# Kernel tuning notes

Measured on AMD Instinct MI355X. Metric: run time of the kernel, lower is better.

## Reference

```python
import jax, jax.numpy as jnp
import numpy as np

B, C, L, H, W = 2, 64, 8, 32, 32

def setup_inputs() -> dict:
    key = jax.random.key(0)
    ks = jax.random.split(key, 10)
    return {
        "q": jax.random.normal(ks[0], (B, C, L, H, W), dtype=jnp.float32),
        "k": jax.random.normal(ks[1], (B, C, L, H, W), dtype=jnp.float32),
        "v": jax.random.normal(ks[2], (B, C, L, H, W), dtype=jnp.float32),
        "wq": jax.random.normal(ks[3], (C,), dtype=jnp.float32) * 0.1,
        "bq": jax.random.normal(ks[4], (1,), dtype=jnp.float32) * 0.1,
        "wk": jax.random.normal(ks[5], (C,), dtype=jnp.float32) * 0.1,
        "bk": jax.random.normal(ks[6], (1,), dtype=jnp.float32) * 0.1,
        "wv": jax.random.normal(ks[7], (C, 3 * C), dtype=jnp.float32) * 0.1,
        "bv": jax.random.normal(ks[8], (C,), dtype=jnp.float32) * 0.1,
        "gamma_x": jax.random.normal(ks[9], (1,), dtype=jnp.float32) * 0.1,
    }


def reference(q, k, v, wq, bq, wk, bk, wv, bv, gamma_x):
    # q,k,v: [B,C,L,H,W]; 1x1x1 conv3d == channel contraction
    Bq, Cq, Lq, Hq, Wq = q.shape
    N = Lq * Hq * Wq
    qf = q.reshape(Bq, Cq, N)
    kf = k.reshape(Bq, Cq, N)
    vf = v.reshape(Bq, Cq, N)
    # query/key conv: C -> 1 channel => [B, N]
    pq = jnp.einsum('bcn,c->bn', qf, wq) + bq  # [B,N]
    pk = jnp.einsum('bcn,c->bn', kf, wk) + bk  # [B,N]
    # energy = bmm([B,N,1],[B,1,N]) = outer product -> [B,N,N]
    energy = pq[:, :, None] * pk[:, None, :]
    attn = jax.nn.softmax(energy, axis=-1)  # softmax over key index n
    # value path: cat(v, q, k) along channels -> [B,3C,N], then 3C -> C conv
    val = jnp.concatenate([vf, qf, kf], axis=1)
    pv = jnp.einsum('bdn,cd->bcn', val, wv) + bv[None, :, None]  # [B,C,N]
    # out[b,c,m] = sum_n pv[b,c,n] * attn[b,m,n]  (bmm with attn^T)
    out = jnp.einsum('bcn,bmn->bcm', pv, attn).reshape(Bq, Cq, Lq, Hq, Wq)
    return gamma_x * out + v
```

## Files before the change

### kernel.cpp

```cpp
#include <hip/hip_runtime.h>


typedef __attribute__((ext_vector_type(8))) __bf16 bf16x8;
typedef __attribute__((ext_vector_type(4))) float  f32x4;

#define NN 8192
#define CC 64
#define NJ 48

__global__ __launch_bounds__(256) void pqpk_kernel(
    const float* __restrict__ q, const float* __restrict__ k,
    const float* __restrict__ wq, const float* __restrict__ bq,
    const float* __restrict__ wk, const float* __restrict__ bk,
    float* __restrict__ pq, float* __restrict__ pk)
{
    int t = threadIdx.x, lane = t & 63, wid = t >> 6;
    int b  = blockIdx.x >> 6;
    int n  = ((blockIdx.x & 63) << 7) + ((wid & 1) << 6) + lane;

    const float* src = (wid < 2) ? q : k;
    const float* wgt = (wid < 2) ? wq : wk;
    float bias       = (wid < 2) ? bq[0] : bk[0];
    float* dst       = (wid < 2) ? pq : pk;

    const float* sp = src + (size_t)b * CC * NN + n;
    float a = 0.f;
    #pragma unroll 8
    for (int d = 0; d < 64; d++) a = fmaf(sp[(size_t)d * NN], wgt[d], a);
    dst[b * NN + n] = a + bias;
}

__global__ __launch_bounds__(256) void fused_kernel(
    const float* __restrict__ q, const float* __restrict__ k,
    const float* __restrict__ v, const float* __restrict__ wv,
    const float* __restrict__ bv, const float* __restrict__ pk,
    float* __restrict__ G, float* __restrict__ T)
{
    __shared__ __align__(16) __bf16 val_sT[64][200];
    __shared__ __align__(16) __bf16 pv_s[64][72];
    __shared__ __align__(16) __bf16 V_s[NJ][72];

    int t = threadIdx.x, lane = t & 63, wid = t >> 6;
    int quad = lane >> 4, cl = lane & 15;
    int b   = blockIdx.x >> 6;
    int nb0 = (blockIdx.x & 63) << 7;
    size_t bo = (size_t)b * CC * NN;

    bf16x8 wvA[6];
    const float* wr = wv + (size_t)(wid * 16 + cl) * 192;
    #pragma unroll
    for (int ks = 0; ks < 6; ks++) {
        f32x4 a0 = *(const f32x4*)(wr + ks * 32 + quad * 8);
        f32x4 a1 = *(const f32x4*)(wr + ks * 32 + quad * 8 + 4);
        #pragma unroll
        for (int e = 0; e < 4; e++) {
            wvA[ks][e]     = (__bf16)a0[e];
            wvA[ks][4 + e] = (__bf16)a1[e];
        }
    }
    float bvr[4];
    #pragma unroll
    for (int r = 0; r < 4; r++) bvr[r] = bv[wid * 16 + quad * 4 + r];

    f32x4 accG[3];
    #pragma unroll
    for (int jt = 0; jt < 3; jt++) accG[jt] = (f32x4){0.f, 0.f, 0.f, 0.f};
    float tsum = 0.f;

    for (int s = 0; s < 2; s++) {
        int n0 = nb0 + s * 64;
        if (wid < 3) {
            int dt = t >> 3, no = t & 7;
            int dbase = dt * 8;
            const float* src = (dbase < 64)  ? (v + bo + (size_t)dbase * NN)
                             : (dbase < 128) ? (q + bo + (size_t)(dbase - 64) * NN)
                                             : (k + bo + (size_t)(dbase - 128) * NN);
            float tile[8][8];
            #pragma unroll
            for (int dd = 0; dd < 8; dd++) {
                f32x4 x0 = *(const f32x4*)(src + (size_t)dd * NN + n0 + no * 8);
                f32x4 x1 = *(const f32x4*)(src + (size_t)dd * NN + n0 + no * 8 + 4);
                #pragma unroll
                for (int e = 0; e < 4; e++) { tile[dd][e] = x0[e]; tile[dd][4 + e] = x1[e]; }
            }
            #pragma unroll
            for (int nn = 0; nn < 8; nn++) {
                bf16x8 wb;
                #pragma unroll
                for (int dd = 0; dd < 8; dd++) wb[dd] = (__bf16)tile[dd][nn];
                *(bf16x8*)&val_sT[no * 8 + nn][dbase] = wb;
            }
        } else {
            float tv = pk[b * NN + n0 + lane];
            float tp = 1.f;
            #pragma unroll
            for (int j = 0; j < NJ; j++) {
                V_s[j][lane] = (__bf16)tp;
                tp *= tv;
            }
        }
        __syncthreads();

        f32x4 accP[4];
        #pragma unroll
        for (int nt = 0; nt < 4; nt++) accP[nt] = (f32x4){0.f, 0.f, 0.f, 0.f};
        #pragma unroll
        for (int ks = 0; ks < 6; ks++)
            #pragma unroll
            for (int nt = 0; nt < 4; nt++) {
                bf16x8 bfr = *(const bf16x8*)&val_sT[nt * 16 + cl][ks * 32 + quad * 8];
                accP[nt] = __builtin_amdgcn_mfma_f32_16x16x32_bf16(wvA[ks], bfr, accP[nt], 0, 0, 0);
            }

        #pragma unroll
        for (int nt = 0; nt < 4; nt++)
            #pragma unroll
            for (int r = 0; r < 4; r++)
                pv_s[wid * 16 + quad * 4 + r][nt * 16 + cl] = (__bf16)(accP[nt][r] + bvr[r]);

        #pragma unroll
        for (int k0 = 0; k0 < 64; k0 += 32) {
            bf16x8 a = *(const bf16x8*)&pv_s[wid * 16 + cl][k0 + quad * 8];
            #pragma unroll
            for (int jt = 0; jt < 3; jt++) {
                bf16x8 bfr = *(const bf16x8*)&V_s[jt * 16 + cl][k0 + quad * 8];
                accG[jt] = __builtin_amdgcn_mfma_f32_16x16x32_bf16(a, bfr, accG[jt], 0, 0, 0);
            }
        }
        if (t < NJ) {
            #pragma unroll
            for (int h = 0; h < 8; h++) {
                bf16x8 vv = *(const bf16x8*)&V_s[t][h * 8];
                #pragma unroll
                for (int e = 0; e < 8; e++) tsum += (float)vv[e];
            }
        }
        __syncthreads();
    }

    #pragma unroll
    for (int jt = 0; jt < 3; jt++)
        #pragma unroll
        for (int r = 0; r < 4; r++)
            atomicAdd(&G[((size_t)b * CC + wid * 16 + quad * 4 + r) * NJ + jt * 16 + cl],
                      accG[jt][r]);
    if (t < NJ) atomicAdd(&T[b * NJ + t], tsum);
}

__global__ __launch_bounds__(256) void eval_kernel(
    const float* __restrict__ pq, const float* __restrict__ G,
    const float* __restrict__ T, const float* __restrict__ v,
    const float* __restrict__ gamma, float* __restrict__ out)
{
    int t = threadIdx.x;
    int b   = blockIdx.x >> 8;
    int mch = (blockIdx.x >> 3) & 31;
    int cg  = blockIdx.x & 7;

    int m = mch * 256 + t;
    float s = pq[b * NN + m];
    const float* Gr = G + ((size_t)b * CC + cg * 8) * NJ;
    const float* Tr = T + b * NJ;

    float acc[8];
    #pragma unroll
    for (int c = 0; c < 8; c++) acc[c] = 0.f;
    float z = 0.f, cj = 1.f;
    #pragma unroll
    for (int j = 0; j < NJ; j++) {
        if (j > 0) cj *= s * (1.0f / (float)j);
        z = fmaf(cj, Tr[j], z);
        #pragma unroll
        for (int c = 0; c < 8; c++) acc[c] = fmaf(cj, Gr[c * NJ + j], acc[c]);
    }
    float gz = gamma[0] / z;

    #pragma unroll
    for (int c = 0; c < 8; c++) {
        size_t idx = ((size_t)b * CC + cg * 8 + c) * NN + m;
        out[idx] = fmaf(gz, acc[c], v[idx]);
    }
}

extern "C" void kernel_launch(void* const* d_in, const int* in_sizes, int n_in,
                              void* d_out, int out_size, void* d_ws, size_t ws_size,
                              hipStream_t stream)
{
    const float* q     = (const float*)d_in[0];
    const float* k     = (const float*)d_in[1];
    const float* v     = (const float*)d_in[2];
    const float* wq    = (const float*)d_in[3];
    const float* bq    = (const float*)d_in[4];
    const float* wk    = (const float*)d_in[5];
    const float* bk    = (const float*)d_in[6];
    const float* wv    = (const float*)d_in[7];
    const float* bv    = (const float*)d_in[8];
    const float* gamma = (const float*)d_in[9];

    float* pqw = (float*)d_ws;
    float* pkw = pqw + 2 * NN;
    float* Gw  = pkw + 2 * NN;
    float* Tw  = Gw + 2 * CC * NJ;

    hipMemsetAsync(Gw, 0, (2 * CC * NJ + 2 * NJ) * sizeof(float), stream);
    pqpk_kernel<<<128, 256, 0, stream>>>(q, k, wq, bq, wk, bk, pqw, pkw);
    fused_kernel<<<128, 256, 0, stream>>>(q, k, v, wv, bv, pkw, Gw, Tw);
    eval_kernel<<<512, 256, 0, stream>>>(pqw, Gw, Tw, v, gamma, (float*)d_out);
}
```

Before: 98.50 us.

## Fold workspace zeroing into pqpk kernel and double grid sizes for parallelism

Removes the separate memset launch by having the projection kernel zero the G/T accumulators. The projection kernel now splits the channel reduction across four waves and combines partial sums in shared memory. The fused kernel processes one 64-column tile per block over 256 blocks instead of looping over two tiles in 128 blocks. The aim is to fill more CUs on the chip and cut launch overhead, at the cost of twice as many atomic adds into G and T.

```diff
diff --git a/kernel.cpp b/kernel.cpp
--- a/kernel.cpp
+++ b/kernel.cpp
@@ -12,22 +12,37 @@
     const float* __restrict__ q, const float* __restrict__ k,
     const float* __restrict__ wq, const float* __restrict__ bq,
     const float* __restrict__ wk, const float* __restrict__ bk,
-    float* __restrict__ pq, float* __restrict__ pk)
-{
+    float* __restrict__ pq, float* __restrict__ pk, float* __restrict__ GT)
+{
+    __shared__ float pqp[4][64], pkp[4][64];
+
     int t = threadIdx.x, lane = t & 63, wid = t >> 6;
-    int b  = blockIdx.x >> 6;
-    int n  = ((blockIdx.x & 63) << 7) + ((wid & 1) << 6) + lane;
-
-    const float* src = (wid < 2) ? q : k;
-    const float* wgt = (wid < 2) ? wq : wk;
-    float bias       = (wid < 2) ? bq[0] : bk[0];
-    float* dst       = (wid < 2) ? pq : pk;
-
-    const float* sp = src + (size_t)b * CC * NN + n;
-    float a = 0.f;
-    #pragma unroll 8
-    for (int d = 0; d < 64; d++) a = fmaf(sp[(size_t)d * NN], wgt[d], a);
-    dst[b * NN + n] = a + bias;
+    int b  = blockIdx.x >> 7;
+    int n0 = (blockIdx.x & 127) << 6;
+    int n  = n0 + lane;
+
+    int gid = blockIdx.x * 256 + t;
+    if (gid < 2 * CC * NJ + 2 * NJ) GT[gid] = 0.f;
+
+    size_t bo = (size_t)b * CC * NN + (size_t)(wid * 16) * NN + n;
+    const float* qp = q + bo;
+    const float* kp = k + bo;
+    float aq = 0.f, ak = 0.f;
+    #pragma unroll
+    for (int d = 0; d < 16; d++) {
+        aq = fmaf(qp[(size_t)d * NN], wq[wid * 16 + d], aq);
+        ak = fmaf(kp[(size_t)d * NN], wk[wid * 16 + d], ak);
+    }
+    pqp[wid][lane] = aq;
+    pkp[wid][lane] = ak;
+    __syncthreads();
+
+    if (t < 64)
+        pq[b * NN + n0 + t] = pqp[0][t] + pqp[1][t] + pqp[2][t] + pqp[3][t] + bq[0];
+    else if (t < 128) {
+        int u = t - 64;
+        pk[b * NN + n0 + u] = pkp[0][u] + pkp[1][u] + pkp[2][u] + pkp[3][u] + bk[0];
+    }
 }
 
 __global__ __launch_bounds__(256) void fused_kernel(
@@ -42,8 +57,8 @@
 
     int t = threadIdx.x, lane = t & 63, wid = t >> 6;
     int quad = lane >> 4, cl = lane & 15;
-    int b   = blockIdx.x >> 6;
-    int nb0 = (blockIdx.x & 63) << 7;
+    int b  = blockIdx.x >> 7;
+    int n0 = (blockIdx.x & 127) << 6;
     size_t bo = (size_t)b * CC * NN;
 
     bf16x8 wvA[6];
@@ -62,80 +77,66 @@
     #pragma unroll
     for (int r = 0; r < 4; r++) bvr[r] = bv[wid * 16 + quad * 4 + r];
 
+    if (wid < 3) {
+        int dt = t >> 3, no = t & 7;
+        int dbase = dt * 8;
+        const float* src = (dbase < 64)  ? (v + bo + (size_t)dbase * NN)
+                         : (dbase < 128) ? (q + bo + (size_t)(dbase - 64) * NN)
+                                         : (k + bo + (size_t)(dbase - 128) * NN);
+        float tile[8][8];
+        #pragma unroll
+        for (int dd = 0; dd < 8; dd++) {
+            f32x4 x0 = *(const f32x4*)(src + (size_t)dd * NN + n0 + no * 8);
+            f32x4 x1 = *(const f32x4*)(src + (size_t)dd * NN + n0 + no * 8 + 4);
+            #pragma unroll
+            for (int e = 0; e < 4; e++) { tile[dd][e] = x0[e]; tile[dd][4 + e] = x1[e]; }
+        }
+        #pragma unroll
+        for (int nn = 0; nn < 8; nn++) {
+            bf16x8 wb;
+            #pragma unroll
+            for (int dd = 0; dd < 8; dd++) wb[dd] = (__bf16)tile[dd][nn];
+            *(bf16x8*)&val_sT[no * 8 + nn][dbase] = wb;
+        }
+    } else {
+        float tv = pk[b * NN + n0 + lane];
+        float tp = 1.f;
+        #pragma unroll
+        for (int j = 0; j < NJ; j++) {
+            V_s[j][lane] = (__bf16)tp;
+            tp *= tv;
+        }
+    }
+    __syncthreads();
+
+    f32x4 accP[4];
+    #pragma unroll
+    for (int nt = 0; nt < 4; nt++) accP[nt] = (f32x4){0.f, 0.f, 0.f, 0.f};
+    #pragma unroll
+    for (int ks = 0; ks < 6; ks++)
+        #pragma unroll
+        for (int nt = 0; nt < 4; nt++) {
+            bf16x8 bfr = *(const bf16x8*)&val_sT[nt * 16 + cl][ks * 32 + quad * 8];
+            accP[nt] = __builtin_amdgcn_mfma_f32_16x16x32_bf16(wvA[ks], bfr, accP[nt], 0, 0, 0);
+        }
+
+    #pragma unroll
+    for (int nt = 0; nt < 4; nt++)
+        #pragma unroll
+        for (int r = 0; r < 4; r++)
+            pv_s[wid * 16 + quad * 4 + r][nt * 16 + cl] = (__bf16)(accP[nt][r] + bvr[r]);
+
     f32x4 accG[3];
     #pragma unroll
     for (int jt = 0; jt < 3; jt++) accG[jt] = (f32x4){0.f, 0.f, 0.f, 0.f};
-    float tsum = 0.f;
-
-    for (int s = 0; s < 2; s++) {
-        int n0 = nb0 + s * 64;
-        if (wid < 3) {
-            int dt = t >> 3, no = t & 7;
-            int dbase = dt * 8;
-            const float* src = (dbase < 64)  ? (v + bo + (size_t)dbase * NN)
-                             : (dbase < 128) ? (q + bo + (size_t)(dbase - 64) * NN)
-                                             : (k + bo + (size_t)(dbase - 128) * NN);
-            float tile[8][8];
-            #pragma unroll
-            for (int dd = 0; dd < 8; dd++) {
-                f32x4 x0 = *(const f32x4*)(src + (size_t)dd * NN + n0 + no * 8);
-                f32x4 x1 = *(const f32x4*)(src + (size_t)dd * NN + n0 + no * 8 + 4);
-                #pragma unroll
-                for (int e = 0; e < 4; e++) { tile[dd][e] = x0[e]; tile[dd][4 + e] = x1[e]; }
-            }
-            #pragma unroll
-            for (int nn = 0; nn < 8; nn++) {
-                bf16x8 wb;
-                #pragma unroll
-                for (int dd = 0; dd < 8; dd++) wb[dd] = (__bf16)tile[dd][nn];
-                *(bf16x8*)&val_sT[no * 8 + nn][dbase] = wb;
-            }
-        } else {
-            float tv = pk[b * NN + n0 + lane];
-            float tp = 1.f;
-            #pragma unroll
-            for (int j = 0; j < NJ; j++) {
-                V_s[j][lane] = (__bf16)tp;
-                tp *= tv;
-            }
-        }
-        __syncthreads();
-
-        f32x4 accP[4];
-        #pragma unroll
-        for (int nt = 0; nt < 4; nt++) accP[nt] = (f32x4){0.f, 0.f, 0.f, 0.f};
-        #pragma unroll
-        for (int ks = 0; ks < 6; ks++)
-            #pragma unroll
-            for (int nt = 0; nt < 4; nt++) {
-                bf16x8 bfr = *(const bf16x8*)&val_sT[nt * 16 + cl][ks * 32 + quad * 8];
-                accP[nt] = __builtin_amdgcn_mfma_f32_16x16x32_bf16(wvA[ks], bfr, accP[nt], 0, 0, 0);
-            }
-
-        #pragma unroll
-        for (int nt = 0; nt < 4; nt++)
-            #pragma unroll
-            for (int r = 0; r < 4; r++)
-                pv_s[wid * 16 + quad * 4 + r][nt * 16 + cl] = (__bf16)(accP[nt][r] + bvr[r]);
-
-        #pragma unroll
-        for (int k0 = 0; k0 < 64; k0 += 32) {
-            bf16x8 a = *(const bf16x8*)&pv_s[wid * 16 + cl][k0 + quad * 8];
-            #pragma unroll
-            for (int jt = 0; jt < 3; jt++) {
-                bf16x8 bfr = *(const bf16x8*)&V_s[jt * 16 + cl][k0 + quad * 8];
-                accG[jt] = __builtin_amdgcn_mfma_f32_16x16x32_bf16(a, bfr, accG[jt], 0, 0, 0);
-            }
-        }
-        if (t < NJ) {
-            #pragma unroll
-            for (int h = 0; h < 8; h++) {
-                bf16x8 vv = *(const bf16x8*)&V_s[t][h * 8];
-                #pragma unroll
-                for (int e = 0; e < 8; e++) tsum += (float)vv[e];
-            }
-        }
-        __syncthreads();
+    #pragma unroll
+    for (int k0 = 0; k0 < 64; k0 += 32) {
+        bf16x8 a = *(const bf16x8*)&pv_s[wid * 16 + cl][k0 + quad * 8];
+        #pragma unroll
+        for (int jt = 0; jt < 3; jt++) {
+            bf16x8 bfr = *(const bf16x8*)&V_s[jt * 16 + cl][k0 + quad * 8];
+            accG[jt] = __builtin_amdgcn_mfma_f32_16x16x32_bf16(a, bfr, accG[jt], 0, 0, 0);
+        }
     }
 
     #pragma unroll
@@ -144,7 +145,17 @@
         for (int r = 0; r < 4; r++)
             atomicAdd(&G[((size_t)b * CC + wid * 16 + quad * 4 + r) * NJ + jt * 16 + cl],
                       accG[jt][r]);
-    if (t < NJ) atomicAdd(&T[b * NJ + t], tsum);
+
+    if (t < NJ) {
+        float tsum = 0.f;
+        #pragma unroll
+        for (int h = 0; h < 8; h++) {
+            bf16x8 vv = *(const bf16x8*)&V_s[t][h * 8];
+            #pragma unroll
+            for (int e = 0; e < 8; e++) tsum += (float)vv[e];
+        }
+        atomicAdd(&T[b * NJ + t], tsum);
+    }
 }
 
 __global__ __launch_bounds__(256) void eval_kernel(
@@ -202,8 +213,7 @@
     float* Gw  = pkw + 2 * NN;
     float* Tw  = Gw + 2 * CC * NJ;
 
-    hipMemsetAsync(Gw, 0, (2 * CC * NJ + 2 * NJ) * sizeof(float), stream);
-    pqpk_kernel<<<128, 256, 0, stream>>>(q, k, wq, bq, wk, bk, pqw, pkw);
-    fused_kernel<<<128, 256, 0, stream>>>(q, k, v, wv, bv, pkw, Gw, Tw);
+    pqpk_kernel<<<256, 256, 0, stream>>>(q, k, wq, bq, wk, bk, pqw, pkw, Gw);
+    fused_kernel<<<256, 256, 0, stream>>>(q, k, v, wv, bv, pkw, Gw, Tw);
     eval_kernel<<<512, 256, 0, stream>>>(pqw, Gw, Tw, v, gamma, (float*)d_out);
 }
```

Measured after the change: 94.86 us. -3.7%, faster.
